# Kernel tuning notes

Measured on AMD Instinct MI355X. Metric: run time of the kernel, lower is better.

## Reference

```python
import jax, jax.numpy as jnp
import numpy as np

B, C, G, P, W, H = 16, 64, 256, 4096, 1024, 256
WQ = W // 4  # wsi_dim // 4 = 256
D = C + G + WQ  # concat dim fed to score MLP = 576


def _init_linear(key, fan_in, fan_out):
    k1, k2 = jax.random.split(key)
    bound = 1.0 / np.sqrt(fan_in)
    w = jax.random.uniform(k1, (fan_in, fan_out), jnp.float32, -bound, bound)
    b = jax.random.uniform(k2, (fan_out,), jnp.float32, -bound, bound)
    return w, b


def setup_inputs() -> dict:
    key = jax.random.key(0)
    ks = jax.random.split(key, 8)
    cx = jax.random.normal(ks[0], (B, C), jnp.float32)
    gx = jax.random.normal(ks[1], (B, G), jnp.float32)
    wx = jax.random.normal(ks[2], (B, P, W), jnp.float32)
    Wc, bc = _init_linear(ks[3], C, C)        # fc_c
    Wg, bg = _init_linear(ks[4], G, G)        # fc_g
    Ww, bw = _init_linear(ks[5], W, WQ)       # fc_w
    W1, b1 = _init_linear(ks[6], D, H)        # FCLayers hidden
    W2, b2 = _init_linear(ks[7], H, 1)        # FCLayers out
    return {"cx": cx, "gx": gx, "wx": wx,
            "Wc": Wc, "bc": bc, "Wg": Wg, "bg": bg, "Ww": Ww, "bw": bw,
            "W1": W1, "b1": b1, "W2": W2, "b2": b2}


def reference(cx, gx, wx, Wc, bc, Wg, bg, Ww, bw, W1, b1, W2, b2):
    # Per-modality projections
    c = cx @ Wc + bc                      # [B, C]
    g = gx @ Wg + bg                      # [B, G]
    w = jnp.einsum('bpw,wq->bpq', wx, Ww) + bw  # [B, P, WQ]
    # Score MLP on concat(c, g, w_i) for every patch, vectorized by
    # splitting W1 rows over the concat blocks (avoids materializing concat):
    W1c, W1g, W1w = W1[:C], W1[C:C + G], W1[C + G:]
    h = jax.nn.relu((c @ W1c + g @ W1g + b1)[:, None, :]
                    + jnp.einsum('bpq,qh->bph', w, W1w))  # [B, P, H]
    scores = h @ W2 + b2                  # [B, P, 1]
    attn = jax.nn.softmax(scores, axis=1)  # softmax over patches
    return jnp.sum(attn * w, axis=1)      # [B, WQ]
```

## Files before the change

kernel.cpp:

```cpp
#include <hip/hip_runtime.h>
#include <hip/hip_bf16.h>

#define B_   16
#define C_   64
#define G_   256
#define P_   4096
#define W_   1024
#define H_   256
#define WQ_  256
#define M_   (B_ * P_)

typedef __attribute__((ext_vector_type(8))) _Float16 f16x8;
typedef __attribute__((ext_vector_type(4))) float    f32x4;

__device__ __forceinline__ float h2f(ushort u) {
    union { ushort u; _Float16 h; } cv; cv.u = u;
    return (float)cv.h;
}

#define GLOAD16(gsrc, ldst)                                                  \
    __builtin_amdgcn_global_load_lds(                                        \
        (const __attribute__((address_space(1))) unsigned int*)(gsrc),       \
        (__attribute__((address_space(3))) unsigned int*)(ldst), 16, 0, 0)

__device__ __forceinline__ void convT_dev(
    const float* __restrict__ src, ushort* __restrict__ dst,
    int K, int N, int blk, float* tile )
{
    const int nb = N >> 6;
    const int k0 = (blk / nb) * 64;
    const int n0 = (blk % nb) * 64;
    const int t = threadIdx.x;
    #pragma unroll
    for (int i = 0; i < 16; ++i) {
        int e = i * 256 + t;
        int kr = e >> 6, nc = e & 63;
        tile[nc * 65 + kr] = src[(size_t)(k0 + kr) * N + n0 + nc];
    }
    __syncthreads();
    #pragma unroll
    for (int i = 0; i < 16; ++i) {
        int e = i * 256 + t;
        int nc = e >> 6, kr = e & 63;
        union { _Float16 h; ushort u; } cv;
        cv.h = (_Float16)tile[nc * 65 + kr];
        dst[(size_t)(n0 + nc) * K + k0 + kr] = cv.u;
    }
}

__global__ __launch_bounds__(256) void setup_kernel(
    const float* __restrict__ Ww,  ushort* __restrict__ WwT,
    const float* __restrict__ W1w, ushort* __restrict__ W1T,
    const float* __restrict__ cx, const float* __restrict__ gx,
    const float* __restrict__ Wc, const float* __restrict__ bc,
    const float* __restrict__ Wg, const float* __restrict__ bg,
    const float* __restrict__ W1, const float* __restrict__ b1,
    float* __restrict__ base_out)
{
    __shared__ float smem[64 * 65];
    const int blk = blockIdx.x;
    if (blk < 64) {
        convT_dev(Ww, WwT, W_, WQ_, blk, smem);
        return;
    }
    if (blk < 80) {
        convT_dev(W1w, W1T, H_, H_, blk - 64, smem);
        return;
    }
    const int b = blk - 80;
    const int t = threadIdx.x;
    float* cxl = smem;
    float* gxl = smem + 64;
    float* cl  = smem + 320;
    float* gl  = smem + 384;

    if (t < C_) cxl[t] = cx[b * C_ + t];
    gxl[t] = gx[b * G_ + t];
    __syncthreads();

    if (t < C_) {
        float acc = bc[t];
        #pragma unroll 4
        for (int i = 0; i < C_; ++i) acc += cxl[i] * Wc[i * C_ + t];
        cl[t] = acc;
    }
    {
        float acc = bg[t];
        #pragma unroll 4
        for (int i = 0; i < G_; ++i) acc += gxl[i] * Wg[i * G_ + t];
        gl[t] = acc;
    }
    __syncthreads();

    float acc = b1[t];
    #pragma unroll 4
    for (int i = 0; i < C_; ++i) acc += cl[i] * W1[i * H_ + t];
    #pragma unroll 4
    for (int i = 0; i < G_; ++i) acc += gl[i] * W1[(C_ + i) * H_ + t];
    base_out[b * H_ + t] = acc;
}

__global__ __launch_bounds__(512, 2) void gemm_w_fused(
    const float* __restrict__ A,
    const ushort* __restrict__ BT,
    const float* __restrict__ bw,
    const ushort* __restrict__ W1T,
    const float* __restrict__ base_,
    const float* __restrict__ W2,
    const float* __restrict__ b2,
    ushort* Cout,
    float* __restrict__ scores)
{
    __shared__ __align__(16) ushort Ah[128 * 64];
    __shared__ __align__(16) ushort Bh[256 * 64];
    __shared__ float red2[4][128];
    const int t = threadIdx.x;
    const int row0 = blockIdx.x * 128;
    const int b = blockIdx.x >> 5;
    const int lane = t & 63, wave = t >> 6;
    const int wm = wave >> 2, wn = wave & 3;
    const int l15 = lane & 15, lq = lane >> 4;

    const int s_ar = t >> 2;
    const int s_ak = (t & 3) * 16;

    const ushort *srcB0, *srcB1, *srcB2, *srcB3;
    char *dstB0, *dstB1, *dstB2, *dstB3;
    {
        const int o0 = t * 16, o1 = o0 + 8192, o2 = o0 + 16384, o3 = o0 + 24576;
        const int c0 = o0 >> 7, c1 = o1 >> 7, c2 = o2 >> 7, c3 = o3 >> 7;
        const int x0 = o0 & 127, x1 = o1 & 127, x2 = o2 & 127, x3 = o3 & 127;
        srcB0 = BT + (size_t)c0 * W_ + ((x0 ^ ((c0 & 7) << 4)) >> 1);
        srcB1 = BT + (size_t)c1 * W_ + ((x1 ^ ((c1 & 7) << 4)) >> 1);
        srcB2 = BT + (size_t)c2 * W_ + ((x2 ^ ((c2 & 7) << 4)) >> 1);
        srcB3 = BT + (size_t)c3 * W_ + ((x3 ^ ((c3 & 7) << 4)) >> 1);
        dstB0 = (char*)Bh + o0; dstB1 = (char*)Bh + o1;
        dstB2 = (char*)Bh + o2; dstB3 = (char*)Bh + o3;
    }

    f32x4 acc[4][4];
    #pragma unroll
    for (int m = 0; m < 4; ++m)
        #pragma unroll
        for (int n = 0; n < 4; ++n) acc[m][n] = (f32x4){0.f, 0.f, 0.f, 0.f};

    for (int k0 = 0; k0 < W_; k0 += 64) {
        if (k0) __syncthreads();
        GLOAD16(srcB0 + k0, dstB0);
        GLOAD16(srcB1 + k0, dstB1);
        GLOAD16(srcB2 + k0, dstB2);
        GLOAD16(srcB3 + k0, dstB3);
        {
            const float* ap = A + (size_t)(row0 + s_ar) * W_ + k0 + s_ak;
            const float4 v0 = *(const float4*)(ap + 0);
            const float4 v1 = *(const float4*)(ap + 4);
            const float4 v2 = *(const float4*)(ap + 8);
            const float4 v3 = *(const float4*)(ap + 12);
            f16x8 h0, h1;
            h0[0] = (_Float16)v0.x; h0[1] = (_Float16)v0.y;
            h0[2] = (_Float16)v0.z; h0[3] = (_Float16)v0.w;
            h0[4] = (_Float16)v1.x; h0[5] = (_Float16)v1.y;
            h0[6] = (_Float16)v1.z; h0[7] = (_Float16)v1.w;
            h1[0] = (_Float16)v2.x; h1[1] = (_Float16)v2.y;
            h1[2] = (_Float16)v2.z; h1[3] = (_Float16)v2.w;
            h1[4] = (_Float16)v3.x; h1[5] = (_Float16)v3.y;
            h1[6] = (_Float16)v3.z; h1[7] = (_Float16)v3.w;
            const int base = s_ar * 128 + s_ak * 2;
            const int swz  = (s_ar & 7) << 4;
            *(f16x8*)((char*)Ah + (base ^ swz)) = h0;
            *(f16x8*)((char*)Ah + ((base + 16) ^ swz)) = h1;
        }
        __syncthreads();

        #pragma unroll
        for (int ks = 0; ks < 2; ++ks) {
            f16x8 af[4], bf[4];
            #pragma unroll
            for (int m = 0; m < 4; ++m) {
                const int r = wm * 64 + m * 16 + l15;
                const int byte = (r * 128 + ks * 64 + lq * 16) ^ ((r & 7) << 4);
                af[m] = *(const f16x8*)((const char*)Ah + byte);
            }
            #pragma unroll
            for (int n = 0; n < 4; ++n) {
                const int c = wn * 64 + n * 16 + l15;
                const int byte = (c * 128 + ks * 64 + lq * 16) ^ ((c & 7) << 4);
                bf[n] = *(const f16x8*)((const char*)Bh + byte);
            }
            #pragma unroll
            for (int m = 0; m < 4; ++m)
                #pragma unroll
                for (int n = 0; n < 4; ++n)
                    acc[m][n] = __builtin_amdgcn_mfma_f32_16x16x32_f16(
                        af[m], bf[n], acc[m][n], 0, 0, 0);
        }
    }

    {
        float bwv[4];
        #pragma unroll
        for (int n = 0; n < 4; ++n) bwv[n] = bw[wn * 64 + n * 16 + l15];
        #pragma unroll
        for (int m = 0; m < 4; ++m)
            #pragma unroll
            for (int reg = 0; reg < 4; ++reg) {
                const size_t r = (size_t)row0 + wm * 64 + m * 16 + lq * 4 + reg;
                #pragma unroll
                for (int n = 0; n < 4; ++n) {
                    union { _Float16 h; ushort u; } cv;
                    cv.h = (_Float16)(acc[m][n][reg] + bwv[n]);
                    Cout[r * WQ_ + wn * 64 + n * 16 + l15] = cv.u;
                }
            }
    }

    __syncthreads();

    f32x4 acc2[4][4];
    #pragma unroll
    for (int m = 0; m < 4; ++m)
        #pragma unroll
        for (int n = 0; n < 4; ++n) acc2[m][n] = (f32x4){0.f, 0.f, 0.f, 0.f};

    for (int k2 = 0; k2 < WQ_; k2 += 32) {
        f16x8 af[4], bf[4];
        #pragma unroll
        for (int m = 0; m < 4; ++m) {
            const size_t r = (size_t)row0 + wm * 64 + m * 16 + l15;
            af[m] = *(const f16x8*)(Cout + r * WQ_ + k2 + lq * 8);
        }
        #pragma unroll
        for (int n = 0; n < 4; ++n) {
            const int c = wn * 64 + n * 16 + l15;
            bf[n] = *(const f16x8*)(W1T + (size_t)c * WQ_ + k2 + lq * 8);
        }
        #pragma unroll
        for (int m = 0; m < 4; ++m)
            #pragma unroll
            for (int n = 0; n < 4; ++n)
                acc2[m][n] = __builtin_amdgcn_mfma_f32_16x16x32_f16(
                    af[m], bf[n], acc2[m][n], 0, 0, 0);
    }

    {
        float basev[4], w2v[4];
        #pragma unroll
        for (int n = 0; n < 4; ++n) {
            const int col = wn * 64 + n * 16 + l15;
            basev[n] = base_[b * H_ + col];
            w2v[n] = W2[col];
        }
        #pragma unroll
        for (int m = 0; m < 4; ++m)
            #pragma unroll
            for (int reg = 0; reg < 4; ++reg) {
                float s = 0.f;
                #pragma unroll
                for (int n = 0; n < 4; ++n) {
                    float h = acc2[m][n][reg] + basev[n];
                    h = fmaxf(h, 0.f);
                    s += h * w2v[n];
                }
                s += __shfl_xor(s, 1, 64);
                s += __shfl_xor(s, 2, 64);
                s += __shfl_xor(s, 4, 64);
                s += __shfl_xor(s, 8, 64);
                if (l15 == 0) red2[wn][wm * 64 + m * 16 + lq * 4 + reg] = s;
            }
        __syncthreads();
        if (t < 128) {
            scores[row0 + t] =
                red2[0][t] + red2[1][t] + red2[2][t] + red2[3][t] + b2[0];
        }
    }
}

__global__ __launch_bounds__(256) void weighted_partial_kernel(
    const ushort* __restrict__ wmat16, const float* __restrict__ scores,
    float* __restrict__ part)
{
    const int blk = blockIdx.x;
    const int b   = blk >> 5;
    const int sl  = blk & 31;
    const int t   = threadIdx.x;
    const int rg  = t >> 5;
    const int q8  = (t & 31) * 8;
    __shared__ float red[8][WQ_];
    __shared__ float mred[4];

    float mv = -1e30f;
    for (int p = t; p < P_; p += 256) mv = fmaxf(mv, scores[b * P_ + p]);
    #pragma unroll
    for (int d = 1; d < 64; d <<= 1) mv = fmaxf(mv, __shfl_xor(mv, d, 64));
    if ((t & 63) == 0) mred[t >> 6] = mv;
    __syncthreads();
    const float m = fmaxf(fmaxf(mred[0], mred[1]), fmaxf(mred[2], mred[3]));

    float acc[8];
    #pragma unroll
    for (int j = 0; j < 8; ++j) acc[j] = 0.f;

    const int p0 = sl * 128 + rg * 16;
    for (int p = p0; p < p0 + 16; ++p) {
        const float e = expf(scores[b * P_ + p] - m);
        const uint4 raw = *(const uint4*)(wmat16 + ((size_t)b * P_ + p) * WQ_ + q8);
        const ushort* u = (const ushort*)&raw;
        #pragma unroll
        for (int j = 0; j < 8; ++j) acc[j] += e * h2f(u[j]);
    }
    #pragma unroll
    for (int j = 0; j < 8; ++j) red[rg][q8 + j] = acc[j];
    __syncthreads();
    float s = 0.f;
    #pragma unroll
    for (int g = 0; g < 8; ++g) s += red[g][t];
    part[(size_t)(b * 32 + sl) * WQ_ + t] = s;
}

__global__ __launch_bounds__(256) void finalize_kernel(
    const float* __restrict__ part, const float* __restrict__ scores,
    float* __restrict__ out)
{
    const int b = blockIdx.x;
    const int t = threadIdx.x;
    __shared__ float mred[4];
    __shared__ float zred[4];

    float mv = -1e30f;
    for (int p = t; p < P_; p += 256) mv = fmaxf(mv, scores[b * P_ + p]);
    #pragma unroll
    for (int d = 1; d < 64; d <<= 1) mv = fmaxf(mv, __shfl_xor(mv, d, 64));
    if ((t & 63) == 0) mred[t >> 6] = mv;
    __syncthreads();
    const float m = fmaxf(fmaxf(mred[0], mred[1]), fmaxf(mred[2], mred[3]));

    float zv = 0.f;
    for (int p = t; p < P_; p += 256) zv += expf(scores[b * P_ + p] - m);
    #pragma unroll
    for (int d = 1; d < 64; d <<= 1) zv += __shfl_xor(zv, d, 64);
    if ((t & 63) == 0) zred[t >> 6] = zv;
    __syncthreads();
    const float z = zred[0] + zred[1] + zred[2] + zred[3];

    float acc = 0.f;
    #pragma unroll
    for (int sl = 0; sl < 32; ++sl) acc += part[(size_t)(b * 32 + sl) * WQ_ + t];
    out[b * WQ_ + t] = acc / z;
}

extern "C" void kernel_launch(void* const* d_in, const int* in_sizes, int n_in,
                              void* d_out, int out_size, void* d_ws, size_t ws_size,
                              hipStream_t stream) {
    const float* cx = (const float*)d_in[0];
    const float* gx = (const float*)d_in[1];
    const float* wx = (const float*)d_in[2];
    const float* Wc = (const float*)d_in[3];
    const float* bc = (const float*)d_in[4];
    const float* Wg = (const float*)d_in[5];
    const float* bg = (const float*)d_in[6];
    const float* Ww = (const float*)d_in[7];
    const float* bw = (const float*)d_in[8];
    const float* W1 = (const float*)d_in[9];
    const float* b1 = (const float*)d_in[10];
    const float* W2 = (const float*)d_in[11];
    const float* b2 = (const float*)d_in[12];
    float* out = (float*)d_out;

    float* ws        = (float*)d_ws;
    ushort* ws_w16   = (ushort*)ws;
    float* ws_scores = ws + (size_t)M_ * WQ_ / 2;
    float* ws_base   = ws_scores + M_;
    float* ws_part   = ws_base + B_ * H_;
    ushort* WwT16    = (ushort*)(ws_part + B_ * 32 * WQ_);
    ushort* W1T16    = WwT16 + (size_t)W_ * WQ_;

    setup_kernel<<<96, 256, 0, stream>>>(
        Ww, WwT16, W1 + (size_t)(C_ + G_) * H_, W1T16,
        cx, gx, Wc, bc, Wg, bg, W1, b1, ws_base);

    gemm_w_fused<<<M_ / 128, 512, 0, stream>>>(
        wx, WwT16, bw, W1T16, ws_base, W2, b2, ws_w16, ws_scores);

    weighted_partial_kernel<<<B_ * 32, 256, 0, stream>>>(ws_w16, ws_scores, ws_part);

    finalize_kernel<<<B_, 256, 0, stream>>>(ws_part, ws_scores, out);
}
```

Before: 184.9 us.

## Load fp32 A tiles directly to LDS and keep projected w tile in LDS

The fp32 activation tile is now staged into LDS with async global-to-LDS loads instead of going through registers with an fp16 conversion before the LDS store. The conversion to fp16 moves to fragment-read time. The projected w tile is also written to a swizzled LDS buffer, so the second GEMM reads it from LDS instead of re-reading the Cout values just written to global memory. Shared memory is unified into a 64KB buffer that is reused across phases, with extra barriers added. The larger LDS footprint may reduce occupancy below the two blocks per CU the launch bounds target, and the conversion work is now repeated per wave.

```diff
diff --git a/kernel.cpp b/kernel.cpp
--- a/kernel.cpp
+++ b/kernel.cpp
@@ -111,9 +111,11 @@
     ushort* Cout,
     float* __restrict__ scores)
 {
-    __shared__ __align__(16) ushort Ah[128 * 64];
-    __shared__ __align__(16) ushort Bh[256 * 64];
-    __shared__ float red2[4][128];
+    __shared__ __align__(16) char smem[65536];
+    float*  Af = (float*)smem;
+    ushort* Bh = (ushort*)(smem + 32768);
+    ushort* wt = (ushort*)smem;
+
     const int t = threadIdx.x;
     const int row0 = blockIdx.x * 128;
     const int b = blockIdx.x >> 5;
@@ -121,19 +123,27 @@
     const int wm = wave >> 2, wn = wave & 3;
     const int l15 = lane & 15, lq = lane >> 4;
 
-    const int s_ar = t >> 2;
-    const int s_ak = (t & 3) * 16;
-
+    const float *srcA0, *srcA1, *srcA2, *srcA3;
+    char *dstA0, *dstA1, *dstA2, *dstA3;
+    {
+        const int o0 = t * 16, o1 = o0 + 8192, o2 = o0 + 16384, o3 = o0 + 24576;
+        const int r0 = o0 >> 8, r1 = o1 >> 8, r2 = o2 >> 8, r3 = o3 >> 8;
+        srcA0 = A + (size_t)(row0 + r0) * W_ + (((o0 & 255) ^ ((r0 & 7) << 4)) >> 2);
+        srcA1 = A + (size_t)(row0 + r1) * W_ + (((o1 & 255) ^ ((r1 & 7) << 4)) >> 2);
+        srcA2 = A + (size_t)(row0 + r2) * W_ + (((o2 & 255) ^ ((r2 & 7) << 4)) >> 2);
+        srcA3 = A + (size_t)(row0 + r3) * W_ + (((o3 & 255) ^ ((r3 & 7) << 4)) >> 2);
+        dstA0 = (char*)Af + o0; dstA1 = (char*)Af + o1;
+        dstA2 = (char*)Af + o2; dstA3 = (char*)Af + o3;
+    }
     const ushort *srcB0, *srcB1, *srcB2, *srcB3;
     char *dstB0, *dstB1, *dstB2, *dstB3;
     {
         const int o0 = t * 16, o1 = o0 + 8192, o2 = o0 + 16384, o3 = o0 + 24576;
         const int c0 = o0 >> 7, c1 = o1 >> 7, c2 = o2 >> 7, c3 = o3 >> 7;
-        const int x0 = o0 & 127, x1 = o1 & 127, x2 = o2 & 127, x3 = o3 & 127;
-        srcB0 = BT + (size_t)c0 * W_ + ((x0 ^ ((c0 & 7) << 4)) >> 1);
-        srcB1 = BT + (size_t)c1 * W_ + ((x1 ^ ((c1 & 7) << 4)) >> 1);
-        srcB2 = BT + (size_t)c2 * W_ + ((x2 ^ ((c2 & 7) << 4)) >> 1);
-        srcB3 = BT + (size_t)c3 * W_ + ((x3 ^ ((c3 & 7) << 4)) >> 1);
+        srcB0 = BT + (size_t)c0 * W_ + (((o0 & 127) ^ ((c0 & 7) << 4)) >> 1);
+        srcB1 = BT + (size_t)c1 * W_ + (((o1 & 127) ^ ((c1 & 7) << 4)) >> 1);
+        srcB2 = BT + (size_t)c2 * W_ + (((o2 & 127) ^ ((c2 & 7) << 4)) >> 1);
+        srcB3 = BT + (size_t)c3 * W_ + (((o3 & 127) ^ ((c3 & 7) << 4)) >> 1);
         dstB0 = (char*)Bh + o0; dstB1 = (char*)Bh + o1;
         dstB2 = (char*)Bh + o2; dstB3 = (char*)Bh + o3;
     }
@@ -146,30 +156,14 @@
 
     for (int k0 = 0; k0 < W_; k0 += 64) {
         if (k0) __syncthreads();
+        GLOAD16(srcA0 + k0, dstA0);
+        GLOAD16(srcA1 + k0, dstA1);
+        GLOAD16(srcA2 + k0, dstA2);
+        GLOAD16(srcA3 + k0, dstA3);
         GLOAD16(srcB0 + k0, dstB0);
         GLOAD16(srcB1 + k0, dstB1);
         GLOAD16(srcB2 + k0, dstB2);
         GLOAD16(srcB3 + k0, dstB3);
-        {
-            const float* ap = A + (size_t)(row0 + s_ar) * W_ + k0 + s_ak;
-            const float4 v0 = *(const float4*)(ap + 0);
-            const float4 v1 = *(const float4*)(ap + 4);
-            const float4 v2 = *(const float4*)(ap + 8);
-            const float4 v3 = *(const float4*)(ap + 12);
-            f16x8 h0, h1;
-            h0[0] = (_Float16)v0.x; h0[1] = (_Float16)v0.y;
-            h0[2] = (_Float16)v0.z; h0[3] = (_Float16)v0.w;
-            h0[4] = (_Float16)v1.x; h0[5] = (_Float16)v1.y;
-            h0[6] = (_Float16)v1.z; h0[7] = (_Float16)v1.w;
-            h1[0] = (_Float16)v2.x; h1[1] = (_Float16)v2.y;
-            h1[2] = (_Float16)v2.z; h1[3] = (_Float16)v2.w;
-            h1[4] = (_Float16)v3.x; h1[5] = (_Float16)v3.y;
-            h1[6] = (_Float16)v3.z; h1[7] = (_Float16)v3.w;
-            const int base = s_ar * 128 + s_ak * 2;
-            const int swz  = (s_ar & 7) << 4;
-            *(f16x8*)((char*)Ah + (base ^ swz)) = h0;
-            *(f16x8*)((char*)Ah + ((base + 16) ^ swz)) = h1;
-        }
         __syncthreads();
 
         #pragma unroll
@@ -178,8 +172,16 @@
             #pragma unroll
             for (int m = 0; m < 4; ++m) {
                 const int r = wm * 64 + m * 16 + l15;
-                const int byte = (r * 128 + ks * 64 + lq * 16) ^ ((r & 7) << 4);
-                af[m] = *(const f16x8*)((const char*)Ah + byte);
+                const int base = r * 256 + ks * 128 + lq * 32;
+                const int swz  = (r & 7) << 4;
+                const f32x4 a0 = *(const f32x4*)((const char*)Af + (base ^ swz));
+                const f32x4 a1 = *(const f32x4*)((const char*)Af + ((base + 16) ^ swz));
+                f16x8 h;
+                h[0] = (_Float16)a0[0]; h[1] = (_Float16)a0[1];
+                h[2] = (_Float16)a0[2]; h[3] = (_Float16)a0[3];
+                h[4] = (_Float16)a1[0]; h[5] = (_Float16)a1[1];
+                h[6] = (_Float16)a1[2]; h[7] = (_Float16)a1[3];
+                af[m] = h;
             }
             #pragma unroll
             for (int n = 0; n < 4; ++n) {
@@ -196,6 +198,7 @@
         }
     }
 
+    __syncthreads();
     {
         float bwv[4];
         #pragma unroll
@@ -204,16 +207,17 @@
         for (int m = 0; m < 4; ++m)
             #pragma unroll
             for (int reg = 0; reg < 4; ++reg) {
-                const size_t r = (size_t)row0 + wm * 64 + m * 16 + lq * 4 + reg;
+                const int rl = wm * 64 + m * 16 + lq * 4 + reg;
                 #pragma unroll
                 for (int n = 0; n < 4; ++n) {
+                    const int col = wn * 64 + n * 16 + l15;
                     union { _Float16 h; ushort u; } cv;
                     cv.h = (_Float16)(acc[m][n][reg] + bwv[n]);
-                    Cout[r * WQ_ + wn * 64 + n * 16 + l15] = cv.u;
+                    Cout[(size_t)(row0 + rl) * WQ_ + col] = cv.u;
+                    *(ushort*)((char*)wt + ((rl * 512 + col * 2) ^ ((rl & 7) << 4))) = cv.u;
                 }
             }
     }
-
     __syncthreads();
 
     f32x4 acc2[4][4];
@@ -226,8 +230,9 @@
         f16x8 af[4], bf[4];
         #pragma unroll
         for (int m = 0; m < 4; ++m) {
-            const size_t r = (size_t)row0 + wm * 64 + m * 16 + l15;
-            af[m] = *(const f16x8*)(Cout + r * WQ_ + k2 + lq * 8);
+            const int r = wm * 64 + m * 16 + l15;
+            const int byte = (r * 512 + (k2 + lq * 8) * 2) ^ ((r & 7) << 4);
+            af[m] = *(const f16x8*)((const char*)wt + byte);
         }
         #pragma unroll
         for (int n = 0; n < 4; ++n) {
@@ -242,7 +247,9 @@
                     af[m], bf[n], acc2[m][n], 0, 0, 0);
     }
 
-    {
+    __syncthreads();
+    {
+        float (*red2)[128] = (float(*)[128])smem;
         float basev[4], w2v[4];
         #pragma unroll
         for (int n = 0; n < 4; ++n) {
```

Result: faster. 177.2 us (-4.2%).
